# Kernel tuning notes

Hardware: AMD Instinct MI355X
Metric: run time of the kernel (lower is better)

The kernel has to match this reference:

```python
import jax, jax.numpy as jnp
import numpy as np

N_COMPANY, N_INDUSTRY, E = 20000, 500, 8192
CC, CI, D, H = 256, 128, 256, 4


def setup_inputs() -> dict:
    key = jax.random.key(0)
    ks = jax.random.split(key, 14)
    p = lambda k, shape: (jax.random.normal(k, shape, jnp.float32) * 0.02)
    company_x = jax.random.normal(ks[0], (N_COMPANY, CC), jnp.float32)
    industry_x = jax.random.normal(ks[1], (N_INDUSTRY, CI), jnp.float32)
    src = jax.random.randint(ks[2], (E,), 0, N_COMPANY)
    tgt = jax.random.randint(ks[3], (E,), 0, N_INDUSTRY)
    edge_index = jnp.stack([src, tgt]).astype(jnp.int64)
    return {
        "company_x": company_x,
        "industry_x": industry_x,
        "edge_index": edge_index,
        "Wc": p(ks[4], (D, CC)), "bc": jnp.zeros((D,), jnp.float32),
        "Wi": p(ks[5], (D, CI)), "bi": jnp.zeros((D,), jnp.float32),
        "w_in": p(ks[6], (3 * D, D)), "b_in": jnp.zeros((3 * D,), jnp.float32),
        "w_out": p(ks[7], (D, D)), "b_out": jnp.zeros((D,), jnp.float32),
        "gamma": jnp.ones((D,), jnp.float32), "beta": jnp.zeros((D,), jnp.float32),
    }


def reference(company_x, industry_x, edge_index, Wc, bc, Wi, bi, w_in, b_in, w_out, b_out, gamma, beta):
    company_h = company_x @ Wc.T + bc          # [N, D]
    industry_h = industry_x @ Wi.T + bi        # [M, D]
    src, tgt = edge_index[0], edge_index[1]
    e = src.shape[0]
    d = company_h.shape[-1]
    hd = d // H

    q_in = company_h[src]                      # [E, D] gather
    kv_in = industry_h[tgt]                    # [E, D] gather

    wq, wk, wv = jnp.split(w_in, 3, axis=0)
    bq, bk, bv = jnp.split(b_in, 3)
    qh = (q_in @ wq.T + bq).reshape(e, H, hd)
    kh = (kv_in @ wk.T + bk).reshape(e, H, hd)
    vh = (kv_in @ wv.T + bv).reshape(e, H, hd)

    scale = 1.0 / jnp.sqrt(jnp.float32(hd))
    scores = jnp.einsum("qhd,khd->hqk", qh * scale, kh)   # [H, E, E]
    attn = jax.nn.softmax(scores, axis=-1)
    ctx = jnp.einsum("hqk,khd->qhd", attn, vh).reshape(e, d)
    attn_out = ctx @ w_out.T + b_out                        # [E, D]

    agg = jax.ops.segment_sum(attn_out, src, num_segments=company_h.shape[0])
    counts = jax.ops.segment_sum(jnp.ones((e,), jnp.float32), src, num_segments=company_h.shape[0])
    pooled = agg / (counts[:, None] + 1e-6)

    out = company_h + pooled
    mean = out.mean(-1, keepdims=True)
    var = out.var(-1, keepdims=True)
    return (out - mean) / jnp.sqrt(var + 1e-5) * gamma + beta
```

## Files before the change

### kernel.cpp

```cpp
#include <hip/hip_runtime.h>

#define E_EDGES 8192
#define N_COMP  20000
#define N_IND   500
#define NKEYS   512

typedef short bf16x8 __attribute__((ext_vector_type(8)));
typedef float f32x4  __attribute__((ext_vector_type(4)));

static __device__ __forceinline__ unsigned short f2bf(float v) {
    unsigned u = __builtin_bit_cast(unsigned, v);
    u = (u + 0x7FFFu + ((u >> 16) & 1u)) >> 16;
    return (unsigned short)u;
}

static __device__ __forceinline__ void cvt8(const float* __restrict__ s,
                                            unsigned short* __restrict__ d) {
    float4 a = *(const float4*)s;
    float4 b = *(const float4*)(s + 4);
    bf16x8 o;
    o[0] = (short)f2bf(a.x); o[1] = (short)f2bf(a.y);
    o[2] = (short)f2bf(a.z); o[3] = (short)f2bf(a.w);
    o[4] = (short)f2bf(b.x); o[5] = (short)f2bf(b.y);
    o[6] = (short)f2bf(b.z); o[7] = (short)f2bf(b.w);
    *(bf16x8*)d = o;
}

static __device__ __forceinline__ bf16x8 cvt8r(const float* __restrict__ s) {
    float4 a = *(const float4*)s;
    float4 b = *(const float4*)(s + 4);
    bf16x8 v;
    v[0] = (short)f2bf(a.x); v[1] = (short)f2bf(a.y);
    v[2] = (short)f2bf(a.z); v[3] = (short)f2bf(a.w);
    v[4] = (short)f2bf(b.x); v[5] = (short)f2bf(b.y);
    v[6] = (short)f2bf(b.z); v[7] = (short)f2bf(b.w);
    return v;
}

#define SWZ(r)   (((r) & 7) << 4)
#define SWZ4(r)  ((((r) >> 1) & 3) << 4)

static __device__ __forceinline__ void stage_f32(const float* src, char* base,
                                                 int sr, int sc) {
    *(bf16x8*)(base + ((sr * 64 + sc * 2) ^ SWZ(sr))) = cvt8r(src);
}

__global__ __launch_bounds__(256) void prep(
    const int* __restrict__ src, const int* __restrict__ tgt,
    const float* __restrict__ Wc, const float* __restrict__ Wi,
    const float* __restrict__ w_out, const float* __restrict__ w_in,
    const float* __restrict__ bc, const float* __restrict__ bi,
    const float* __restrict__ b_in,
    float* __restrict__ csrc, float* __restrict__ ctgt,
    unsigned short* __restrict__ Wc_bf, unsigned short* __restrict__ wout_bf,
    unsigned short* __restrict__ WcT_bf, unsigned short* __restrict__ Wi_bf,
    unsigned short* __restrict__ wkv_bf, float* __restrict__ beff)
{
    const int bid = blockIdx.x, tid = threadIdx.x;
    if (bid < 32) {
        int e = bid * 256 + tid;
        atomicAdd(&csrc[src[e]], 1.0f);
        atomicAdd(&ctgt[tgt[e]], 1.0f);
    } else if (bid < 64) {
        long i = ((long)(bid - 32) * 256 + tid) * 8;
        cvt8(Wc + i, Wc_bf + i);
    } else if (bid < 96) {
        long i = ((long)(bid - 64) * 256 + tid) * 8;
        cvt8(w_out + i, wout_bf + i);
    } else if (bid < 128) {
        long o = ((long)(bid - 96) * 256 + tid) * 8;
        int c = (int)(o >> 8), d0 = (int)(o & 255);
        bf16x8 v;
#pragma unroll
        for (int j = 0; j < 8; j++) v[j] = (short)f2bf(Wc[(long)(d0 + j) * 256 + c]);
        *(bf16x8*)(WcT_bf + o) = v;
    } else if (bid < 144) {
        long i = ((long)(bid - 128) * 256 + tid) * 8;
        cvt8(Wi + i, Wi_bf + i);
    } else if (bid < 208) {
        long i = ((long)(bid - 144) * 256 + tid) * 8;
        cvt8(w_in + 65536 + i, wkv_bf + i);
    } else {
        int gi = (bid - 208) * 256 + tid;
        int e = gi >> 2, q = gi & 3;
        const float* base = (e < 256) ? bc : bi;
        const float* wr = w_in + (long)e * 256 + q * 64;
        const float* br = base + q * 64;
        float s = 0.f;
#pragma unroll
        for (int j = 0; j < 64; j += 4) {
            float4 w4 = *(const float4*)(wr + j);
            float4 b4 = *(const float4*)(br + j);
            s += w4.x * b4.x + w4.y * b4.y + w4.z * b4.z + w4.w * b4.w;
        }
        s += __shfl_xor(s, 1);
        s += __shfl_xor(s, 2);
        if (q == 0) beff[e] = s + b_in[e];
    }
}

__global__ __launch_bounds__(256) void fusedW(
    const float* __restrict__ w_in, const unsigned short* __restrict__ WcT_bf,
    const float* __restrict__ industry_x, const unsigned short* __restrict__ Wi_bf,
    const unsigned short* __restrict__ wkv_bf, const float* __restrict__ beff,
    const float* __restrict__ ctgt, const float* __restrict__ csrc,
    unsigned short* __restrict__ Wcq_bf, unsigned short* __restrict__ Kbuf,
    unsigned short* __restrict__ VTg,
    float* __restrict__ cntT, int* __restrict__ list, int* __restrict__ nlist)
{
    const int bid = blockIdx.x;
    if (bid >= 20) {
        int i = (bid - 20) * 256 + threadIdx.x;
        if (i < NKEYS) cntT[(i & 15) * 32 + (i >> 4)] = ctgt[i];
        if (i < N_COMP && csrc[i] > 0.f) {
            int k = atomicAdd(nlist, 1);
            list[k] = i;
        }
        return;
    }

    __shared__ char lds[48 * 1024];
    const int t = threadIdx.x, wv = t >> 6, lane = t & 63;
    const int g = lane >> 4, ln = lane & 15;
    const int sr = t >> 2, sc = (t & 3) * 8;

    if (bid < 4) {
        char* ab = lds;
        char* wb = lds + 4 * 1024;
        const int bm = bid * 64;
        f32x4 acc[16];
#pragma unroll
        for (int i = 0; i < 16; i++) acc[i] = (f32x4){0.f, 0.f, 0.f, 0.f};
        const float* aptr = w_in + (long)(bm + sr) * 256 + sc;
        for (int kc = 0; kc < 256; kc += 32) {
            __syncthreads();
            stage_f32(aptr + kc, ab, sr, sc);
#pragma unroll
            for (int p = 0; p < 4; p++) {
                int r = p * 64 + sr;
                *(bf16x8*)(wb + ((r * 64 + sc * 2) ^ SWZ(r))) =
                    *(const bf16x8*)(WcT_bf + (long)r * 256 + kc + sc);
            }
            __syncthreads();
            int ar = wv * 16 + ln;
            bf16x8 af = *(bf16x8*)(ab + ((ar * 64 + g * 16) ^ SWZ(ar)));
#pragma unroll
            for (int nj = 0; nj < 16; nj++) {
                int wr = nj * 16 + ln;
                bf16x8 bf = *(bf16x8*)(wb + ((wr * 64 + g * 16) ^ SWZ(wr)));
                acc[nj] = __builtin_amdgcn_mfma_f32_16x16x32_bf16(af, bf, acc[nj], 0, 0, 0);
            }
        }
#pragma unroll
        for (int nj = 0; nj < 16; nj++)
#pragma unroll
            for (int r = 0; r < 4; r++)
                Wcq_bf[(long)(bm + wv * 16 + g * 4 + r) * 256 + nj * 16 + ln] =
                    f2bf(acc[nj][r]);
        return;
    }

    const int rg = (bid - 4) >> 1, colh = (bid - 4) & 1;
    char* ab  = lds;
    char* wb1 = lds + 4 * 1024;
    char* ihb = lds + 16 * 1024;
    char* wb2 = lds;

    {
        f32x4 a1[16];
#pragma unroll
        for (int i = 0; i < 16; i++) a1[i] = (f32x4){0.f, 0.f, 0.f, 0.f};
        int arow = rg * 64 + sr; if (arow > N_IND - 1) arow = N_IND - 1;
        const float* aptr = industry_x + (long)arow * 128 + sc;
        for (int kc = 0; kc < 128; kc += 32) {
            __syncthreads();
            stage_f32(aptr + kc, ab, sr, sc);
#pragma unroll
            for (int p = 0; p < 4; p++) {
                int r = p * 64 + sr;
                *(bf16x8*)(wb1 + ((r * 64 + sc * 2) ^ SWZ(r))) =
                    *(const bf16x8*)(Wi_bf + (long)r * 128 + kc + sc);
            }
            __syncthreads();
            int ar = wv * 16 + ln;
            bf16x8 af = *(bf16x8*)(ab + ((ar * 64 + g * 16) ^ SWZ(ar)));
#pragma unroll
            for (int nj = 0; nj < 16; nj++) {
                int wr = nj * 16 + ln;
                bf16x8 bf = *(bf16x8*)(wb1 + ((wr * 64 + g * 16) ^ SWZ(wr)));
                a1[nj] = __builtin_amdgcn_mfma_f32_16x16x32_bf16(af, bf, a1[nj], 0, 0, 0);
            }
        }
        __syncthreads();
#pragma unroll
        for (int nj = 0; nj < 16; nj++)
#pragma unroll
            for (int r = 0; r < 4; r++) {
                int row = wv * 16 + g * 4 + r, col = nj * 16 + ln;
                *(unsigned short*)(ihb + ((row * 512 + col * 2) ^ SWZ(row))) =
                    f2bf(a1[nj][r]);
            }
    }
    __syncthreads();

    if (colh == 0) {
        f32x4 a2[16];
#pragma unroll
        for (int i = 0; i < 16; i++) a2[i] = (f32x4){0.f, 0.f, 0.f, 0.f};
        for (int kc = 0; kc < 256; kc += 32) {
            __syncthreads();
#pragma unroll
            for (int p = 0; p < 4; p++) {
                int r = p * 64 + sr;
                *(bf16x8*)(wb2 + ((r * 64 + sc * 2) ^ SWZ(r))) =
                    *(const bf16x8*)(wkv_bf + (long)r * 256 + kc + sc);
            }
            __syncthreads();
            int row = wv * 16 + ln;
            bf16x8 af = *(bf16x8*)(ihb + ((row * 512 + (kc + g * 8) * 2) ^ SWZ(row)));
#pragma unroll
            for (int nj = 0; nj < 16; nj++) {
                int wr = nj * 16 + ln;
                bf16x8 bf = *(bf16x8*)(wb2 + ((wr * 64 + g * 16) ^ SWZ(wr)));
                a2[nj] = __builtin_amdgcn_mfma_f32_16x16x32_bf16(af, bf, a2[nj], 0, 0, 0);
            }
        }
#pragma unroll
        for (int nj = 0; nj < 16; nj++)
#pragma unroll
            for (int r = 0; r < 4; r++) {
                int R = rg * 64 + wv * 16 + g * 4 + r, n = nj * 16 + ln;
                Kbuf[(long)R * 256 + n] = f2bf(a2[nj][r] + beff[256 + n]);
            }
    } else {
        const unsigned short* wp = wkv_bf + 65536;
        f32x4 a2[16];
#pragma unroll
        for (int i = 0; i < 16; i++) a2[i] = (f32x4){0.f, 0.f, 0.f, 0.f};
        for (int kc = 0; kc < 256; kc += 32) {
            __syncthreads();
#pragma unroll
            for (int p = 0; p < 4; p++) {
                int r = p * 64 + sr;
                *(bf16x8*)(wb2 + ((r * 64 + sc * 2) ^ SWZ(r))) =
                    *(const bf16x8*)(wp + (long)r * 256 + kc + sc);
            }
            __syncthreads();
#pragma unroll
            for (int mi = 0; mi < 4; mi++) {
                int arow = wv * 64 + mi * 16 + ln;
                bf16x8 af = *(bf16x8*)(wb2 + ((arow * 64 + g * 16) ^ SWZ(arow)));
#pragma unroll
                for (int t4 = 0; t4 < 4; t4++) {
                    int brow = t4 * 16 + ln;
                    bf16x8 bfr = *(bf16x8*)(ihb + ((brow * 512 + (kc + g * 8) * 2) ^ SWZ(brow)));
                    a2[mi * 4 + t4] = __builtin_amdgcn_mfma_f32_16x16x32_bf16(af, bfr, a2[mi * 4 + t4], 0, 0, 0);
                }
            }
        }
#pragma unroll
        for (int mi = 0; mi < 4; mi++)
#pragma unroll
            for (int t4 = 0; t4 < 4; t4++)
#pragma unroll
                for (int r = 0; r < 4; r++) {
                    int nrow = wv * 64 + mi * 16 + g * 4 + r;
                    VTg[(long)nrow * 512 + rg * 64 + t4 * 16 + ln] =
                        f2bf(a2[mi * 4 + t4][r] + beff[512 + nrow]);
                }
    }
}

__global__ __launch_bounds__(256) void qproj(
    const float* __restrict__ company_x, const int* __restrict__ list,
    const int* __restrict__ nlist, const unsigned short* __restrict__ Wcq,
    const float* __restrict__ beff, unsigned short* __restrict__ Qb)
{
    const int M = *nlist;
    const int bm = blockIdx.x * 64;
    if (bm >= M) return;

    __shared__ unsigned short As[64 * 32];
    __shared__ unsigned short Ws[256 * 32];
    char* abase = (char*)As;
    char* wbase = (char*)Ws;

    const int t = threadIdx.x;
    const int wv = t >> 6, lane = t & 63, g = lane >> 4, ln = lane & 15;

    f32x4 acc[16];
#pragma unroll
    for (int i = 0; i < 16; i++) acc[i] = (f32x4){0.f, 0.f, 0.f, 0.f};

    const int sr = t >> 2;
    const int sc = (t & 3) * 8;
    int mrow = bm + sr; if (mrow > M - 1) mrow = M - 1;
    const float* aptr = company_x + (long)list[mrow] * 256 + sc;

    for (int kc = 0; kc < 256; kc += 32) {
        __syncthreads();
        stage_f32(aptr + kc, abase, sr, sc);
#pragma unroll
        for (int p = 0; p < 4; p++) {
            int r = p * 64 + sr;
            *(bf16x8*)(wbase + ((r * 64 + sc * 2) ^ SWZ(r))) =
                *(const bf16x8*)(Wcq + (long)r * 256 + kc + sc);
        }
        __syncthreads();
        const int ar = wv * 16 + ln;
        bf16x8 af = *(bf16x8*)(abase + ((ar * 64 + g * 16) ^ SWZ(ar)));
#pragma unroll
        for (int nj = 0; nj < 16; nj++) {
            int wr = nj * 16 + ln;
            bf16x8 bf = *(bf16x8*)(wbase + ((wr * 64 + g * 16) ^ SWZ(wr)));
            acc[nj] = __builtin_amdgcn_mfma_f32_16x16x32_bf16(af, bf, acc[nj], 0, 0, 0);
        }
    }
#pragma unroll
    for (int nj = 0; nj < 16; nj++) {
        int n = nj * 16 + ln;
        float bv = beff[n];
#pragma unroll
        for (int r = 0; r < 4; r++) {
            int m = bm + wv * 16 + g * 4 + r;
            if (m < M)
                Qb[(long)m * 256 + n] = f2bf((acc[nj][r] + bv) * 0.125f);
        }
    }
}

__global__ __launch_bounds__(256) void megattn(
    const unsigned short* __restrict__ Qb,
    const unsigned short* __restrict__ Kbuf,
    const unsigned short* __restrict__ VTg,
    const float* __restrict__ cntT,
    const int* __restrict__ list, const int* __restrict__ nlist,
    unsigned short* __restrict__ ctx_sc)
{
    const int M = *nlist;
    const int bm = blockIdx.x * 16;
    if (bm >= M) return;

    __shared__ char lds[16384];
    const int t = threadIdx.x, h = t >> 6, lane = t & 63;
    const int g = lane >> 4, ln = lane & 15;
    char* pbase = lds + h * 4096;

    bf16x8 qf0, qf1;
    {
        int qrow = bm + ln; if (qrow > M - 1) qrow = M - 1;
        const unsigned short* qp = Qb + (long)qrow * 256 + h * 64 + g * 8;
        qf0 = *(const bf16x8*)(qp);
        qf1 = *(const bf16x8*)(qp + 32);
    }

    f32x4 acc[4];
#pragma unroll
    for (int i = 0; i < 4; i++) acc[i] = (f32x4){0.f, 0.f, 0.f, 0.f};
    float mreg[4] = {-1e30f, -1e30f, -1e30f, -1e30f};
    float lreg[4] = {0.f, 0.f, 0.f, 0.f};

#pragma unroll
    for (int tile = 0; tile < 2; tile++) {
        float cnt[16];
        {
            const float* cp = cntT + ln * 32 + tile * 16;
#pragma unroll
            for (int j4 = 0; j4 < 4; j4++) {
                float4 c4 = *(const float4*)(cp + j4 * 4);
                cnt[j4 * 4 + 0] = c4.x; cnt[j4 * 4 + 1] = c4.y;
                cnt[j4 * 4 + 2] = c4.z; cnt[j4 * 4 + 3] = c4.w;
            }
        }

        f32x4 S[8][2];
#pragma unroll
        for (int half = 0; half < 2; half++) {
            bf16x8 k0r[4][2], k1r[4][2];
#pragma unroll
            for (int c4 = 0; c4 < 4; c4++)
#pragma unroll
                for (int sub = 0; sub < 2; sub++) {
                    const unsigned short* kr = Kbuf +
                        (long)(tile * 256 + (half * 4 + c4) * 32 + sub * 16 + ln) * 256 + h * 64 + g * 8;
                    k0r[c4][sub] = *(const bf16x8*)(kr);
                    k1r[c4][sub] = *(const bf16x8*)(kr + 32);
                }
#pragma unroll
            for (int c4 = 0; c4 < 4; c4++)
#pragma unroll
                for (int sub = 0; sub < 2; sub++) {
                    f32x4 s = (f32x4){0.f, 0.f, 0.f, 0.f};
                    s = __builtin_amdgcn_mfma_f32_16x16x32_bf16(qf0, k0r[c4][sub], s, 0, 0, 0);
                    s = __builtin_amdgcn_mfma_f32_16x16x32_bf16(qf1, k1r[c4][sub], s, 0, 0, 0);
                    S[half * 4 + c4][sub] = s;
                }
        }

        bf16x8 vr[2][2][4];
#pragma unroll
        for (int j = 0; j < 2; j++)
#pragma unroll
            for (int t4 = 0; t4 < 4; t4++)
                vr[0][j][t4] = *(const bf16x8*)(
                    VTg + (long)(h * 64 + t4 * 16 + ln) * 512 + tile * 256 + j * 32 + g * 8);

        float tm[4] = {-1e30f, -1e30f, -1e30f, -1e30f};
#pragma unroll
        for (int c = 0; c < 8; c++)
#pragma unroll
            for (int sub = 0; sub < 2; sub++)
#pragma unroll
                for (int r = 0; r < 4; r++) tm[r] = fmaxf(tm[r], S[c][sub][r]);
#pragma unroll
        for (int st = 1; st < 16; st <<= 1)
#pragma unroll
            for (int r = 0; r < 4; r++) tm[r] = fmaxf(tm[r], __shfl_xor(tm[r], st));

        float corr[4];
#pragma unroll
        for (int r = 0; r < 4; r++) {
            float mn = fmaxf(mreg[r], tm[r]);
            corr[r] = __expf(mreg[r] - mn);
            mreg[r] = mn;
        }

        float ps[4] = {0.f, 0.f, 0.f, 0.f};
#pragma unroll
        for (int c = 0; c < 8; c++)
#pragma unroll
            for (int sub = 0; sub < 2; sub++) {
                float cv = cnt[c * 2 + sub];
#pragma unroll
                for (int r = 0; r < 4; r++) {
                    float p = cv * __expf(S[c][sub][r] - mreg[r]);
                    S[c][sub][r] = p;
                    ps[r] += p;
                }
            }
#pragma unroll
        for (int st = 1; st < 16; st <<= 1)
#pragma unroll
            for (int r = 0; r < 4; r++) ps[r] += __shfl_xor(ps[r], st);
#pragma unroll
        for (int r = 0; r < 4; r++) lreg[r] = lreg[r] * corr[r] + ps[r];
#pragma unroll
        for (int i = 0; i < 4; i++)
#pragma unroll
            for (int r = 0; r < 4; r++) acc[i][r] *= corr[r];

#pragma unroll
        for (int grp = 0; grp < 4; grp++) {
            if (grp < 3) {
#pragma unroll
                for (int j = 0; j < 2; j++)
#pragma unroll
                    for (int t4 = 0; t4 < 4; t4++)
                        vr[(grp + 1) & 1][j][t4] = *(const bf16x8*)(
                            VTg + (long)(h * 64 + t4 * 16 + ln) * 512 +
                            tile * 256 + ((grp + 1) * 2 + j) * 32 + g * 8);
            }
#pragma unroll
            for (int j = 0; j < 2; j++) {
                int c = grp * 2 + j;
                char* pb = pbase + (c & 3) * 1024;
#pragma unroll
                for (int sub = 0; sub < 2; sub++)
#pragma unroll
                    for (int r = 0; r < 4; r++) {
                        int row = g * 4 + r;
                        *(unsigned short*)(pb + ((row * 64 + (sub * 16 + ln) * 2) ^ SWZ4(row))) =
                            f2bf(S[c][sub][r]);
                    }
                bf16x8 pa = *(bf16x8*)(pb + ((ln * 64 + g * 16) ^ SWZ4(ln)));
#pragma unroll
                for (int t4 = 0; t4 < 4; t4++)
                    acc[t4] = __builtin_amdgcn_mfma_f32_16x16x32_bf16(
                        pa, vr[grp & 1][j][t4], acc[t4], 0, 0, 0);
            }
        }
    }

#pragma unroll
    for (int r = 0; r < 4; r++) {
        int R = bm + g * 4 + r;
        if (R < M) {
            long base = (long)list[R] * 256 + h * 64;
#pragma unroll
            for (int t4 = 0; t4 < 4; t4++)
                ctx_sc[base + t4 * 16 + ln] = f2bf(acc[t4][r] / lreg[r]);
        }
    }
}

__global__ __launch_bounds__(256) void gemm_ln(
    const float* __restrict__ A, const unsigned short* __restrict__ ctx_sc,
    const unsigned short* __restrict__ W, const float* __restrict__ bias,
    const unsigned short* __restrict__ wout, const float* __restrict__ b_out,
    const float* __restrict__ csrc, const float* __restrict__ gamma,
    const float* __restrict__ beta, float* __restrict__ out, int M)
{
    __shared__ unsigned short As[64 * 32];
    __shared__ unsigned short Cs[64 * 32];
    __shared__ unsigned short Ws[256 * 32];
    __shared__ unsigned short Os[256 * 32];
    char* abase = (char*)As;
    char* cbase = (char*)Cs;
    char* wbase = (char*)Ws;
    char* obase = (char*)Os;

    const int bm = blockIdx.x * 64;
    const int t = threadIdx.x;
    const int wv = t >> 6, lane = t & 63, g = lane >> 4, ln = lane & 15;

    f32x4 acc[16], oacc[16];
#pragma unroll
    for (int i = 0; i < 16; i++) {
        acc[i]  = (f32x4){0.f, 0.f, 0.f, 0.f};
        oacc[i] = (f32x4){0.f, 0.f, 0.f, 0.f};
    }

    const int sr = t >> 2;
    const int sc = (t & 3) * 8;
    int arow = bm + sr; if (arow > M - 1) arow = M - 1;
    const float* aptr = A + (long)arow * 256 + sc;
    const unsigned short* cptr = ctx_sc + (long)arow * 256 + sc;

    for (int kc = 0; kc < 256; kc += 32) {
        __syncthreads();
        stage_f32(aptr + kc, abase, sr, sc);
        *(bf16x8*)(cbase + ((sr * 64 + sc * 2) ^ SWZ(sr))) =
            *(const bf16x8*)(cptr + kc);
#pragma unroll
        for (int p = 0; p < 4; p++) {
            int r = p * 64 + sr;
            *(bf16x8*)(wbase + ((r * 64 + sc * 2) ^ SWZ(r))) =
                *(const bf16x8*)(W + (long)r * 256 + kc + sc);
            *(bf16x8*)(obase + ((r * 64 + sc * 2) ^ SWZ(r))) =
                *(const bf16x8*)(wout + (long)r * 256 + kc + sc);
        }
        __syncthreads();

        const int ar = wv * 16 + ln;
        bf16x8 af = *(bf16x8*)(abase + ((ar * 64 + g * 16) ^ SWZ(ar)));
        bf16x8 cf = *(bf16x8*)(cbase + ((ar * 64 + g * 16) ^ SWZ(ar)));
#pragma unroll
        for (int nj = 0; nj < 16; nj++) {
            int wr = nj * 16 + ln;
            bf16x8 bf = *(bf16x8*)(wbase + ((wr * 64 + g * 16) ^ SWZ(wr)));
            bf16x8 of = *(bf16x8*)(obase + ((wr * 64 + g * 16) ^ SWZ(wr)));
            acc[nj]  = __builtin_amdgcn_mfma_f32_16x16x32_bf16(af, bf, acc[nj], 0, 0, 0);
            oacc[nj] = __builtin_amdgcn_mfma_f32_16x16x32_bf16(cf, of, oacc[nj], 0, 0, 0);
        }
    }

#pragma unroll
    for (int r = 0; r < 4; r++) {
        int R = bm + wv * 16 + g * 4 + r;
        bool valid = R < M;
        int Rc = valid ? R : 0;
        float cntv = csrc[Rc];
        float factor = (valid && cntv > 0.f) ? cntv / (cntv + 1e-6f) : 0.f;

        float v[16];
        float sum = 0.f, sq = 0.f;
#pragma unroll
        for (int nj = 0; nj < 16; nj++) {
            int n = nj * 16 + ln;
            float x = acc[nj][r] + bias[n] + factor * (oacc[nj][r] + b_out[n]);
            v[nj] = x;
            sum += x;
            sq  += x * x;
        }
#pragma unroll
        for (int st = 1; st < 16; st <<= 1) {
            sum += __shfl_xor(sum, st);
            sq  += __shfl_xor(sq,  st);
        }
        float mean = sum * (1.0f / 256.0f);
        float var  = sq * (1.0f / 256.0f) - mean * mean;
        float rstd = rsqrtf(var + 1e-5f);
        if (valid) {
#pragma unroll
            for (int nj = 0; nj < 16; nj++) {
                int n = nj * 16 + ln;
                out[(long)R * 256 + n] = (v[nj] - mean) * rstd * gamma[n] + beta[n];
            }
        }
    }
}

extern "C" void kernel_launch(void* const* d_in, const int* in_sizes, int n_in,
                              void* d_out, int out_size, void* d_ws, size_t ws_size,
                              hipStream_t stream)
{
    const float* company_x  = (const float*)d_in[0];
    const float* industry_x = (const float*)d_in[1];
    const int*   edge       = (const int*)d_in[2];
    const float* Wc         = (const float*)d_in[3];
    const float* bc         = (const float*)d_in[4];
    const float* Wi         = (const float*)d_in[5];
    const float* bi         = (const float*)d_in[6];
    const float* w_in       = (const float*)d_in[7];
    const float* b_in       = (const float*)d_in[8];
    const float* w_out      = (const float*)d_in[9];
    const float* b_out      = (const float*)d_in[10];
    const float* gamma      = (const float*)d_in[11];
    const float* beta       = (const float*)d_in[12];
    float* out = (float*)d_out;

    const int* src = edge;
    const int* tgt = edge + E_EDGES;

    float* wf = (float*)d_ws;
    size_t o = 0;
    unsigned short* Wc_bf   = (unsigned short*)(wf + o); o += 32768;
    unsigned short* wout_bf = (unsigned short*)(wf + o); o += 32768;
    unsigned short* WcT_bf  = (unsigned short*)(wf + o); o += 32768;
    unsigned short* Wi_bf   = (unsigned short*)(wf + o); o += 16384;
    unsigned short* wkv_bf  = (unsigned short*)(wf + o); o += 65536;
    unsigned short* Wcq_bf  = (unsigned short*)(wf + o); o += 32768;
    unsigned short* Kbuf    = (unsigned short*)(wf + o); o += 65536;
    unsigned short* VTg     = (unsigned short*)(wf + o); o += 65536;
    unsigned short* Qb      = (unsigned short*)(wf + o); o += (size_t)E_EDGES * 128;
    unsigned short* ctx_sc  = (unsigned short*)(wf + o); o += (size_t)N_COMP * 128;
    float* beff             = wf + o; o += 768;
    float* cntT             = wf + o; o += NKEYS;
    int*   list             = (int*)(wf + o); o += E_EDGES;
    float* csrc             = wf + o; o += N_COMP;
    float* ctgt             = wf + o; o += NKEYS;
    int*   nlist            = (int*)(wf + o); o += 4;

    hipMemsetAsync(csrc, 0, (N_COMP + NKEYS + 4) * sizeof(float), stream);

    prep<<<dim3(220), dim3(256), 0, stream>>>(
        src, tgt, Wc, Wi, w_out, w_in, bc, bi, b_in,
        csrc, ctgt, Wc_bf, wout_bf, WcT_bf, Wi_bf, wkv_bf, beff);

    fusedW<<<dim3(99), dim3(256), 0, stream>>>(
        w_in, WcT_bf, industry_x, Wi_bf, wkv_bf, beff, ctgt, csrc,
        Wcq_bf, Kbuf, VTg, cntT, list, nlist);

    qproj<<<dim3(128), dim3(256), 0, stream>>>(
        company_x, list, nlist, Wcq_bf, beff, Qb);

    megattn<<<dim3(512), dim3(256), 0, stream>>>(
        Qb, Kbuf, VTg, cntT, list, nlist, ctx_sc);

    gemm_ln<<<dim3((N_COMP + 63) / 64), dim3(256), 0, stream>>>(
        company_x, ctx_sc, Wc_bf, bc, wout_bf, b_out,
        csrc, gamma, beta, out, N_COMP);
}
```

Before: 112.2 us.

## Split attention keys across two blocks and move output projection to merge kernel

The attention kernel now splits the 512 keys into two halves, one per block, doubling the grid. Each block writes unnormalized fp32 partial context plus per-row max and sum. A new merge kernel combines the two halves with log-sum-exp rescaling and applies the w_out projection only to the unique source rows, writing fp32 pooled rows. gemm_ln drops its second GEMM over all 20000 rows and instead reads pooled. The cost is an extra launch, fp32 partial buffers, and a full-size pooled read in gemm_ln, including rows that were never written.

Result: slower. 121.6 us (+8.4%).

```diff
diff --git a/kernel.cpp b/kernel.cpp
--- a/kernel.cpp
+++ b/kernel.cpp
@@ -334,11 +334,12 @@
     const unsigned short* __restrict__ Kbuf,
     const unsigned short* __restrict__ VTg,
     const float* __restrict__ cntT,
-    const int* __restrict__ list, const int* __restrict__ nlist,
-    unsigned short* __restrict__ ctx_sc)
+    const int* __restrict__ nlist,
+    float* __restrict__ accP, float* __restrict__ mP, float* __restrict__ lP)
 {
     const int M = *nlist;
-    const int bm = blockIdx.x * 16;
+    const int qt = blockIdx.x >> 1, ks = blockIdx.x & 1;
+    const int bm = qt * 16;
     if (bm >= M) return;
 
     __shared__ char lds[16384];
@@ -354,203 +355,249 @@
         qf1 = *(const bf16x8*)(qp + 32);
     }
 
+    float cnt[16];
+    {
+        const float* cp = cntT + ln * 32 + ks * 16;
+#pragma unroll
+        for (int j4 = 0; j4 < 4; j4++) {
+            float4 c4 = *(const float4*)(cp + j4 * 4);
+            cnt[j4 * 4 + 0] = c4.x; cnt[j4 * 4 + 1] = c4.y;
+            cnt[j4 * 4 + 2] = c4.z; cnt[j4 * 4 + 3] = c4.w;
+        }
+    }
+
+    f32x4 S[8][2];
+#pragma unroll
+    for (int half = 0; half < 2; half++) {
+        bf16x8 k0r[4][2], k1r[4][2];
+#pragma unroll
+        for (int c4 = 0; c4 < 4; c4++)
+#pragma unroll
+            for (int sub = 0; sub < 2; sub++) {
+                const unsigned short* kr = Kbuf +
+                    (long)(ks * 256 + (half * 4 + c4) * 32 + sub * 16 + ln) * 256 + h * 64 + g * 8;
+                k0r[c4][sub] = *(const bf16x8*)(kr);
+                k1r[c4][sub] = *(const bf16x8*)(kr + 32);
+            }
+#pragma unroll
+        for (int c4 = 0; c4 < 4; c4++)
+#pragma unroll
+            for (int sub = 0; sub < 2; sub++) {
+                f32x4 s = (f32x4){0.f, 0.f, 0.f, 0.f};
+                s = __builtin_amdgcn_mfma_f32_16x16x32_bf16(qf0, k0r[c4][sub], s, 0, 0, 0);
+                s = __builtin_amdgcn_mfma_f32_16x16x32_bf16(qf1, k1r[c4][sub], s, 0, 0, 0);
+                S[half * 4 + c4][sub] = s;
+            }
+    }
+
+    bf16x8 vr[2][2][4];
+#pragma unroll
+    for (int j = 0; j < 2; j++)
+#pragma unroll
+        for (int t4 = 0; t4 < 4; t4++)
+            vr[0][j][t4] = *(const bf16x8*)(
+                VTg + (long)(h * 64 + t4 * 16 + ln) * 512 + ks * 256 + j * 32 + g * 8);
+
+    float tm[4] = {-1e30f, -1e30f, -1e30f, -1e30f};
+#pragma unroll
+    for (int c = 0; c < 8; c++)
+#pragma unroll
+        for (int sub = 0; sub < 2; sub++)
+#pragma unroll
+            for (int r = 0; r < 4; r++) tm[r] = fmaxf(tm[r], S[c][sub][r]);
+#pragma unroll
+    for (int st = 1; st < 16; st <<= 1)
+#pragma unroll
+        for (int r = 0; r < 4; r++) tm[r] = fmaxf(tm[r], __shfl_xor(tm[r], st));
+
+    float ps[4] = {0.f, 0.f, 0.f, 0.f};
+#pragma unroll
+    for (int c = 0; c < 8; c++)
+#pragma unroll
+        for (int sub = 0; sub < 2; sub++) {
+            float cv = cnt[c * 2 + sub];
+#pragma unroll
+            for (int r = 0; r < 4; r++) {
+                float p = cv * __expf(S[c][sub][r] - tm[r]);
+                S[c][sub][r] = p;
+                ps[r] += p;
+            }
+        }
+#pragma unroll
+    for (int st = 1; st < 16; st <<= 1)
+#pragma unroll
+        for (int r = 0; r < 4; r++) ps[r] += __shfl_xor(ps[r], st);
+
     f32x4 acc[4];
 #pragma unroll
     for (int i = 0; i < 4; i++) acc[i] = (f32x4){0.f, 0.f, 0.f, 0.f};
-    float mreg[4] = {-1e30f, -1e30f, -1e30f, -1e30f};
-    float lreg[4] = {0.f, 0.f, 0.f, 0.f};
-
-#pragma unroll
-    for (int tile = 0; tile < 2; tile++) {
-        float cnt[16];
-        {
-            const float* cp = cntT + ln * 32 + tile * 16;
-#pragma unroll
-            for (int j4 = 0; j4 < 4; j4++) {
-                float4 c4 = *(const float4*)(cp + j4 * 4);
-                cnt[j4 * 4 + 0] = c4.x; cnt[j4 * 4 + 1] = c4.y;
-                cnt[j4 * 4 + 2] = c4.z; cnt[j4 * 4 + 3] = c4.w;
-            }
-        }
-
-        f32x4 S[8][2];
-#pragma unroll
-        for (int half = 0; half < 2; half++) {
-            bf16x8 k0r[4][2], k1r[4][2];
-#pragma unroll
-            for (int c4 = 0; c4 < 4; c4++)
-#pragma unroll
-                for (int sub = 0; sub < 2; sub++) {
-                    const unsigned short* kr = Kbuf +
-                        (long)(tile * 256 + (half * 4 + c4) * 32 + sub * 16 + ln) * 256 + h * 64 + g * 8;
-                    k0r[c4][sub] = *(const bf16x8*)(kr);
-                    k1r[c4][sub] = *(const bf16x8*)(kr + 32);
+#pragma unroll
+    for (int grp = 0; grp < 4; grp++) {
+        if (grp < 3) {
+#pragma unroll
+            for (int j = 0; j < 2; j++)
+#pragma unroll
+                for (int t4 = 0; t4 < 4; t4++)
+                    vr[(grp + 1) & 1][j][t4] = *(const bf16x8*)(
+                        VTg + (long)(h * 64 + t4 * 16 + ln) * 512 +
+                        ks * 256 + ((grp + 1) * 2 + j) * 32 + g * 8);
+        }
+#pragma unroll
+        for (int j = 0; j < 2; j++) {
+            int c = grp * 2 + j;
+            char* pb = pbase + (c & 3) * 1024;
+#pragma unroll
+            for (int sub = 0; sub < 2; sub++)
+#pragma unroll
+                for (int r = 0; r < 4; r++) {
+                    int row = g * 4 + r;
+                    *(unsigned short*)(pb + ((row * 64 + (sub * 16 + ln) * 2) ^ SWZ4(row))) =
+                        f2bf(S[c][sub][r]);
                 }
-#pragma unroll
-            for (int c4 = 0; c4 < 4; c4++)
-#pragma unroll
-                for (int sub = 0; sub < 2; sub++) {
-                    f32x4 s = (f32x4){0.f, 0.f, 0.f, 0.f};
-                    s = __builtin_amdgcn_mfma_f32_16x16x32_bf16(qf0, k0r[c4][sub], s, 0, 0, 0);
-                    s = __builtin_amdgcn_mfma_f32_16x16x32_bf16(qf1, k1r[c4][sub], s, 0, 0, 0);
-                    S[half * 4 + c4][sub] = s;
-                }
-        }
-
-        bf16x8 vr[2][2][4];
-#pragma unroll
-        for (int j = 0; j < 2; j++)
+            bf16x8 pa = *(bf16x8*)(pb + ((ln * 64 + g * 16) ^ SWZ4(ln)));
 #pragma unroll
             for (int t4 = 0; t4 < 4; t4++)
-                vr[0][j][t4] = *(const bf16x8*)(
-                    VTg + (long)(h * 64 + t4 * 16 + ln) * 512 + tile * 256 + j * 32 + g * 8);
-
-        float tm[4] = {-1e30f, -1e30f, -1e30f, -1e30f};
-#pragma unroll
-        for (int c = 0; c < 8; c++)
-#pragma unroll
-            for (int sub = 0; sub < 2; sub++)
-#pragma unroll
-                for (int r = 0; r < 4; r++) tm[r] = fmaxf(tm[r], S[c][sub][r]);
-#pragma unroll
-        for (int st = 1; st < 16; st <<= 1)
-#pragma unroll
-            for (int r = 0; r < 4; r++) tm[r] = fmaxf(tm[r], __shfl_xor(tm[r], st));
-
-        float corr[4];
+                acc[t4] = __builtin_amdgcn_mfma_f32_16x16x32_bf16(
+                    pa, vr[grp & 1][j][t4], acc[t4], 0, 0, 0);
+        }
+    }
+
+#pragma unroll
+    for (int t4 = 0; t4 < 4; t4++)
 #pragma unroll
         for (int r = 0; r < 4; r++) {
-            float mn = fmaxf(mreg[r], tm[r]);
-            corr[r] = __expf(mreg[r] - mn);
-            mreg[r] = mn;
-        }
-
-        float ps[4] = {0.f, 0.f, 0.f, 0.f};
-#pragma unroll
-        for (int c = 0; c < 8; c++)
-#pragma unroll
-            for (int sub = 0; sub < 2; sub++) {
-                float cv = cnt[c * 2 + sub];
-#pragma unroll
-                for (int r = 0; r < 4; r++) {
-                    float p = cv * __expf(S[c][sub][r] - mreg[r]);
-                    S[c][sub][r] = p;
-                    ps[r] += p;
-                }
-            }
-#pragma unroll
-        for (int st = 1; st < 16; st <<= 1)
-#pragma unroll
-            for (int r = 0; r < 4; r++) ps[r] += __shfl_xor(ps[r], st);
-#pragma unroll
-        for (int r = 0; r < 4; r++) lreg[r] = lreg[r] * corr[r] + ps[r];
-#pragma unroll
-        for (int i = 0; i < 4; i++)
-#pragma unroll
-            for (int r = 0; r < 4; r++) acc[i][r] *= corr[r];
-
-#pragma unroll
-        for (int grp = 0; grp < 4; grp++) {
-            if (grp < 3) {
-#pragma unroll
-                for (int j = 0; j < 2; j++)
-#pragma unroll
-                    for (int t4 = 0; t4 < 4; t4++)
-                        vr[(grp + 1) & 1][j][t4] = *(const bf16x8*)(
-                            VTg + (long)(h * 64 + t4 * 16 + ln) * 512 +
-                            tile * 256 + ((grp + 1) * 2 + j) * 32 + g * 8);
-            }
-#pragma unroll
-            for (int j = 0; j < 2; j++) {
-                int c = grp * 2 + j;
-                char* pb = pbase + (c & 3) * 1024;
-#pragma unroll
-                for (int sub = 0; sub < 2; sub++)
-#pragma unroll
-                    for (int r = 0; r < 4; r++) {
-                        int row = g * 4 + r;
-                        *(unsigned short*)(pb + ((row * 64 + (sub * 16 + ln) * 2) ^ SWZ4(row))) =
-                            f2bf(S[c][sub][r]);
-                    }
-                bf16x8 pa = *(bf16x8*)(pb + ((ln * 64 + g * 16) ^ SWZ4(ln)));
-#pragma unroll
-                for (int t4 = 0; t4 < 4; t4++)
-                    acc[t4] = __builtin_amdgcn_mfma_f32_16x16x32_bf16(
-                        pa, vr[grp & 1][j][t4], acc[t4], 0, 0, 0);
-            }
-        }
-    }
-
+            int R = bm + g * 4 + r;
+            if (R < M)
+                accP[((long)ks * E_EDGES + R) * 256 + h * 64 + t4 * 16 + ln] =
+                    acc[t4][r];
+        }
+    if (ln == 0) {
+#pragma unroll
+        for (int r = 0; r < 4; r++) {
+            int R = bm + g * 4 + r;
+            if (R < M) {
+                mP[(ks * 4 + h) * E_EDGES + R] = tm[r];
+                lP[(ks * 4 + h) * E_EDGES + R] = ps[r];
+            }
+        }
+    }
+}
+
+__global__ __launch_bounds__(256, 2) void merge_out(
+    const float* __restrict__ accP, const float* __restrict__ mP,
+    const float* __restrict__ lP,
+    const unsigned short* __restrict__ wout, const float* __restrict__ b_out,
+    const int* __restrict__ list, const int* __restrict__ nlist,
+    float* __restrict__ pooled)
+{
+    const int M = *nlist;
+    const int bm = blockIdx.x * 16;
+    if (bm >= M) return;
+
+    __shared__ char lds[8192];
+    const int t = threadIdx.x, h = t >> 6, lane = t & 63;
+    const int g = lane >> 4, ln = lane & 15;
+    char* qb = lds + h * 2048;
+
+    float s0[4], s1[4];
+    int gr[4];
 #pragma unroll
     for (int r = 0; r < 4; r++) {
         int R = bm + g * 4 + r;
-        if (R < M) {
-            long base = (long)list[R] * 256 + h * 64;
-#pragma unroll
-            for (int t4 = 0; t4 < 4; t4++)
-                ctx_sc[base + t4 * 16 + ln] = f2bf(acc[t4][r] / lreg[r]);
+        gr[r] = (R > M - 1) ? (M - 1) : R;
+        float m0 = mP[(0 + h) * E_EDGES + gr[r]];
+        float m1 = mP[(4 + h) * E_EDGES + gr[r]];
+        float l0 = lP[(0 + h) * E_EDGES + gr[r]];
+        float l1 = lP[(4 + h) * E_EDGES + gr[r]];
+        float mn = fmaxf(m0, m1);
+        float c0 = __expf(m0 - mn), c1 = __expf(m1 - mn);
+        float inv = 1.0f / (l0 * c0 + l1 * c1);
+        s0[r] = c0 * inv;
+        s1[r] = c1 * inv;
+    }
+#pragma unroll
+    for (int t4 = 0; t4 < 4; t4++)
+#pragma unroll
+        for (int r = 0; r < 4; r++) {
+            int col = h * 64 + t4 * 16 + ln;
+            float a0 = accP[((long)0 * E_EDGES + gr[r]) * 256 + col];
+            float a1 = accP[((long)1 * E_EDGES + gr[r]) * 256 + col];
+            float ctx = a0 * s0[r] + a1 * s1[r];
+            int row = g * 4 + r, c2 = t4 * 16 + ln;
+            *(unsigned short*)(qb + ((row * 128 + c2 * 2) ^ SWZ(row))) = f2bf(ctx);
+        }
+    __syncthreads();
+
+    f32x4 oa[4];
+#pragma unroll
+    for (int i = 0; i < 4; i++) oa[i] = (f32x4){0.f, 0.f, 0.f, 0.f};
+#pragma unroll
+    for (int kc = 0; kc < 256; kc += 32) {
+        int hs = kc >> 6;
+        int off = (kc & 63) + g * 8;
+        bf16x8 af = *(bf16x8*)(lds + hs * 2048 + ((ln * 128 + off * 2) ^ SWZ(ln)));
+#pragma unroll
+        for (int nj = 0; nj < 4; nj++) {
+            bf16x8 bf = *(const bf16x8*)(wout + (long)(h * 64 + nj * 16 + ln) * 256 + kc + g * 8);
+            oa[nj] = __builtin_amdgcn_mfma_f32_16x16x32_bf16(af, bf, oa[nj], 0, 0, 0);
+        }
+    }
+#pragma unroll
+    for (int nj = 0; nj < 4; nj++) {
+        int n = h * 64 + nj * 16 + ln;
+        float bv = b_out[n];
+#pragma unroll
+        for (int r = 0; r < 4; r++) {
+            int R = bm + g * 4 + r;
+            if (R < M)
+                pooled[(long)list[R] * 256 + n] = oa[nj][r] + bv;
         }
     }
 }
 
 __global__ __launch_bounds__(256) void gemm_ln(
-    const float* __restrict__ A, const unsigned short* __restrict__ ctx_sc,
-    const unsigned short* __restrict__ W, const float* __restrict__ bias,
-    const unsigned short* __restrict__ wout, const float* __restrict__ b_out,
-    const float* __restrict__ csrc, const float* __restrict__ gamma,
-    const float* __restrict__ beta, float* __restrict__ out, int M)
+    const float* __restrict__ A, const unsigned short* __restrict__ W,
+    const float* __restrict__ bias,
+    const float* __restrict__ pooled, const float* __restrict__ csrc,
+    const float* __restrict__ gamma, const float* __restrict__ beta,
+    float* __restrict__ out, int M, int K)
 {
     __shared__ unsigned short As[64 * 32];
-    __shared__ unsigned short Cs[64 * 32];
     __shared__ unsigned short Ws[256 * 32];
-    __shared__ unsigned short Os[256 * 32];
     char* abase = (char*)As;
-    char* cbase = (char*)Cs;
     char* wbase = (char*)Ws;
-    char* obase = (char*)Os;
 
     const int bm = blockIdx.x * 64;
     const int t = threadIdx.x;
     const int wv = t >> 6, lane = t & 63, g = lane >> 4, ln = lane & 15;
 
-    f32x4 acc[16], oacc[16];
-#pragma unroll
-    for (int i = 0; i < 16; i++) {
-        acc[i]  = (f32x4){0.f, 0.f, 0.f, 0.f};
-        oacc[i] = (f32x4){0.f, 0.f, 0.f, 0.f};
-    }
+    f32x4 acc[16];
+#pragma unroll
+    for (int i = 0; i < 16; i++) acc[i] = (f32x4){0.f, 0.f, 0.f, 0.f};
 
     const int sr = t >> 2;
     const int sc = (t & 3) * 8;
     int arow = bm + sr; if (arow > M - 1) arow = M - 1;
-    const float* aptr = A + (long)arow * 256 + sc;
-    const unsigned short* cptr = ctx_sc + (long)arow * 256 + sc;
-
-    for (int kc = 0; kc < 256; kc += 32) {
+    const float* aptr = A + (long)arow * K + sc;
+
+    for (int kc = 0; kc < K; kc += 32) {
         __syncthreads();
         stage_f32(aptr + kc, abase, sr, sc);
-        *(bf16x8*)(cbase + ((sr * 64 + sc * 2) ^ SWZ(sr))) =
-            *(const bf16x8*)(cptr + kc);
 #pragma unroll
         for (int p = 0; p < 4; p++) {
             int r = p * 64 + sr;
             *(bf16x8*)(wbase + ((r * 64 + sc * 2) ^ SWZ(r))) =
-                *(const bf16x8*)(W + (long)r * 256 + kc + sc);
-            *(bf16x8*)(obase + ((r * 64 + sc * 2) ^ SWZ(r))) =
-                *(const bf16x8*)(wout + (long)r * 256 + kc + sc);
+                *(const bf16x8*)(W + (long)r * K + kc + sc);
         }
         __syncthreads();
 
         const int ar = wv * 16 + ln;
         bf16x8 af = *(bf16x8*)(abase + ((ar * 64 + g * 16) ^ SWZ(ar)));
-        bf16x8 cf = *(bf16x8*)(cbase + ((ar * 64 + g * 16) ^ SWZ(ar)));
 #pragma unroll
         for (int nj = 0; nj < 16; nj++) {
             int wr = nj * 16 + ln;
             bf16x8 bf = *(bf16x8*)(wbase + ((wr * 64 + g * 16) ^ SWZ(wr)));
-            bf16x8 of = *(bf16x8*)(obase + ((wr * 64 + g * 16) ^ SWZ(wr)));
-            acc[nj]  = __builtin_amdgcn_mfma_f32_16x16x32_bf16(af, bf, acc[nj], 0, 0, 0);
-            oacc[nj] = __builtin_amdgcn_mfma_f32_16x16x32_bf16(cf, of, oacc[nj], 0, 0, 0);
+            acc[nj] = __builtin_amdgcn_mfma_f32_16x16x32_bf16(af, bf, acc[nj], 0, 0, 0);
         }
     }
 
@@ -567,7 +614,7 @@
 #pragma unroll
         for (int nj = 0; nj < 16; nj++) {
             int n = nj * 16 + ln;
-            float x = acc[nj][r] + bias[n] + factor * (oacc[nj][r] + b_out[n]);
+            float x = acc[nj][r] + bias[n] + factor * pooled[(long)Rc * 256 + n];
             v[nj] = x;
             sum += x;
             sq  += x * x;
@@ -623,7 +670,10 @@
     unsigned short* Kbuf    = (unsigned short*)(wf + o); o += 65536;
     unsigned short* VTg     = (unsigned short*)(wf + o); o += 65536;
     unsigned short* Qb      = (unsigned short*)(wf + o); o += (size_t)E_EDGES * 128;
-    unsigned short* ctx_sc  = (unsigned short*)(wf + o); o += (size_t)N_COMP * 128;
+    float* pooled           = wf + o; o += (size_t)N_COMP * 256;
+    float* accP             = wf + o; o += (size_t)2 * E_EDGES * 256;
+    float* mPb              = wf + o; o += (size_t)8 * E_EDGES;
+    float* lPb              = wf + o; o += (size_t)8 * E_EDGES;
     float* beff             = wf + o; o += 768;
     float* cntT             = wf + o; o += NKEYS;
     int*   list             = (int*)(wf + o); o += E_EDGES;
@@ -644,10 +694,12 @@
     qproj<<<dim3(128), dim3(256), 0, stream>>>(
         company_x, list, nlist, Wcq_bf, beff, Qb);
 
-    megattn<<<dim3(512), dim3(256), 0, stream>>>(
-        Qb, Kbuf, VTg, cntT, list, nlist, ctx_sc);
+    megattn<<<dim3(1024), dim3(256), 0, stream>>>(
+        Qb, Kbuf, VTg, cntT, nlist, accP, mPb, lPb);
+
+    merge_out<<<dim3(512), dim3(256), 0, stream>>>(
+        accP, mPb, lPb, wout_bf, b_out, list, nlist, pooled);
 
     gemm_ln<<<dim3((N_COMP + 63) / 64), dim3(256), 0, stream>>>(
-        company_x, ctx_sc, Wc_bf, bc, wout_bf, b_out,
-        csrc, gamma, beta, out, N_COMP);
-}
+        company_x, Wc_bf, bc, pooled, csrc, gamma, beta, out, N_COMP, 256);
+}
```
